# Performance work log

Hardware: AMD Instinct MI355X
Metric: run time of the kernel (lower is better)

Reference implementation:

```python
import jax, jax.numpy as jnp
import numpy as np

N = 200000   # num nodes
E = 2500000  # num edges
H = 32       # hidden_dim
EPS = 1e-5   # BatchNorm eps


def _gcn_conv(x, W, b, src, dst, norm):
    # GCNConv: D^{-1/2}(A+I)D^{-1/2} X W + b  (self-loops folded in via norm^2 term)
    h = x @ W                                   # [N, H_out]
    coef = norm[src] * norm[dst]                # [E]
    msg = h[src] * coef[:, None]                # [E, H_out] -- dominant HBM traffic
    agg = jax.ops.segment_sum(msg, dst, num_segments=N)
    agg = agg + h * (norm * norm)[:, None]      # self-loop contribution
    return agg + b


def _bn(x, gamma, beta):
    # BatchNorm1d in training mode: batch statistics over the node dimension
    m = jnp.mean(x, axis=0)
    v = jnp.var(x, axis=0)
    return gamma * (x - m) * jax.lax.rsqrt(v + EPS) + beta


def setup_inputs() -> dict:
    key = jax.random.key(0)
    ks = jax.random.split(key, 12)
    x = jax.random.uniform(ks[0], (N, 1), dtype=jnp.float32) * 50.0  # degree-like feature
    edge_index = jax.random.randint(ks[1], (2, E), 0, N, dtype=jnp.int64)
    edge_attr = jax.random.normal(ks[2], (E,), dtype=jnp.float32)
    s = 0.1
    return {
        'x': x, 'edge_index': edge_index, 'edge_attr': edge_attr,
        'W1': jax.random.normal(ks[3], (1, H), dtype=jnp.float32) * s,
        'b1': jnp.zeros((H,), jnp.float32),
        'g1': jnp.ones((H,), jnp.float32), 'be1': jnp.zeros((H,), jnp.float32),
        'W2': jax.random.normal(ks[4], (H, H), dtype=jnp.float32) * s,
        'b2': jnp.zeros((H,), jnp.float32),
        'g2': jnp.ones((H,), jnp.float32), 'be2': jnp.zeros((H,), jnp.float32),
        'W3': jax.random.normal(ks[5], (H, H), dtype=jnp.float32) * s,
        'b3': jnp.zeros((H,), jnp.float32),
        'g3': jnp.ones((H,), jnp.float32), 'be3': jnp.zeros((H,), jnp.float32),
        'fcW': jax.random.normal(ks[6], (H, 1), dtype=jnp.float32) * s,
        'fcb': jnp.zeros((1,), jnp.float32),
    }


def reference(x, edge_index, edge_attr, W1, b1, g1, be1, W2, b2, g2, be2,
              W3, b3, g3, be3, fcW, fcb):
    src, dst = edge_index[0], edge_index[1]
    # symmetric normalization from degrees of A + I
    deg = jax.ops.segment_sum(jnp.ones((E,), x.dtype), dst, num_segments=N) + 1.0
    norm = jax.lax.rsqrt(deg)                   # deg^{-1/2}, [N]

    h = jax.nn.relu(_bn(_gcn_conv(x, W1, b1, src, dst, norm), g1, be1))
    h = jax.nn.relu(_bn(_gcn_conv(h, W2, b2, src, dst, norm), g2, be2))
    h = jax.nn.relu(_bn(_gcn_conv(h, W3, b3, src, dst, norm), g3, be3))
    # dropout is identity in eval / deterministic reference
    return h @ fcW + fcb                        # [N, 1]
```

## Files before the change

kernel.cpp:

```cpp
#include <hip/hip_runtime.h>
#include <hip/hip_bf16.h>
#include <hip/hip_fp16.h>

#define N_NODES 200000
#define N_EDGES 2500000
#define HID 32
#define BN_EPS 1e-5f

#define BKT_SHIFT 10
#define B_BKT ((N_NODES + 1023) / 1024)
#define PAD 16
#define CAPB 14336
#define EDGES_PER_BLK 8192
#define NB_SCAT ((N_EDGES + EDGES_PER_BLK - 1) / EDGES_PER_BLK)

#define SBANK 4096
#define SSTR 16
#define S1SUM 0
#define S1SQ  16
#define L2SUM 32
#define L2SQ  544
#define L3SUM 1056
#define L3SQ  1568

#define NBN32 6250
#define NBL2  3125
#define ITL2  2
#define NBH   3125

typedef float nfloat4 __attribute__((ext_vector_type(4)));

__device__ __forceinline__ void atomAddF(float* p, float v) {
    unsafeAtomicAdd(p, v);
}

__device__ __forceinline__ void ntStore4(float* p, float a, float b, float c, float d) {
    nfloat4 v = {a, b, c, d};
    __builtin_nontemporal_store(v, (nfloat4*)p);
}

__global__ void k_init(int* __restrict__ bcur16, float* __restrict__ stats) {
    int i = blockIdx.x * blockDim.x + threadIdx.x;
    if (i < B_BKT * PAD) bcur16[i] = 0;
    if (i < 4 * SBANK) stats[i] = 0.0f;
}

__global__ void __launch_bounds__(1024)
k_scatter(const int* __restrict__ ei, int* __restrict__ bcur16,
          unsigned int* __restrict__ ebuf) {
    __shared__ int lh[B_BKT], lbase[B_BKT], lc[B_BKT];
    int t = threadIdx.x;
    if (t < B_BKT) { lh[t] = 0; lc[t] = 0; }
    __syncthreads();
    int base = blockIdx.x * EDGES_PER_BLK;
    int sv[8], dv[8];
#pragma unroll
    for (int k = 0; k < 8; k++) {
        int e = base + k * 1024 + t;
        if (e < N_EDGES) {
            sv[k] = ei[e];
            dv[k] = ei[N_EDGES + e];
            atomicAdd(&lh[dv[k] >> BKT_SHIFT], 1);
        } else dv[k] = -1;
    }
    __syncthreads();
    if (t < B_BKT) lbase[t] = lh[t] ? atomicAdd(&bcur16[t * PAD], lh[t]) : 0;
    __syncthreads();
#pragma unroll
    for (int k = 0; k < 8; k++) {
        if (dv[k] >= 0) {
            int b = dv[k] >> BKT_SHIFT;
            int loc = atomicAdd(&lc[b], 1);
            ebuf[(size_t)b * CAPB + lbase[b] + loc] =
                ((unsigned)(dv[k] & 1023) << 18) | (unsigned)sv[k];
        }
    }
}

__global__ void __launch_bounds__(1024)
k_bucket(const unsigned int* __restrict__ ebuf, const int* __restrict__ bcur16,
         const float* __restrict__ x, int* __restrict__ rowbeg,
         int* __restrict__ cntg, float* __restrict__ norm,
         float* __restrict__ xp, int* __restrict__ csrc) {
    __shared__ int hist[1024], rbase[1024];
    __shared__ int wsum[16];
    int b = blockIdx.x;
    int t = threadIdx.x;
    int lane = t & 63, wv = t >> 6;
    int count = bcur16[b * PAD];
    size_t ebase = (size_t)b * CAPB;
    int nbase = b << BKT_SHIFT;
    hist[t] = 0;
    __syncthreads();
    for (int i = t; i < count; i += 1024)
        atomicAdd(&hist[ebuf[ebase + i] >> 18], 1);
    __syncthreads();
    int v = hist[t];
    int val = v;
#pragma unroll
    for (int off = 1; off < 64; off <<= 1) {
        int nn = __shfl_up(val, off);
        if (lane >= off) val += nn;
    }
    if (lane == 63) wsum[wv] = val;
    __syncthreads();
    if (t < 16) {
        int wval = wsum[t];
        int wincl = wval;
#pragma unroll
        for (int off = 1; off < 16; off <<= 1) {
            int nn = __shfl_up(wincl, off, 16);
            if (t >= off) wincl += nn;
        }
        wsum[t] = wincl - wval;
    }
    __syncthreads();
    int excl = (val - v) + wsum[wv];
    int rb = b * CAPB + excl;
    rbase[t] = rb;
    int n = nbase + t;
    if (n < N_NODES) {
        rowbeg[n] = rb;
        cntg[n] = v;
        float nm = rsqrtf((float)v + 1.0f);
        norm[n] = nm;
        xp[n] = x[n] * nm;
    }
    __syncthreads();
    hist[t] = 0;
    __syncthreads();
    for (int i = t; i < count; i += 1024) {
        unsigned int w = ebuf[ebase + i];
        int ld = w >> 18;
        int loc = atomicAdd(&hist[ld], 1);
        csrc[rbase[ld] + loc] = (int)(w & 0x3FFFFu);
    }
}

__global__ void __launch_bounds__(256)
k_gather1(const int* __restrict__ rowbeg, const int* __restrict__ cntg,
          const int* __restrict__ csrc, const float* __restrict__ xp,
          const float* __restrict__ norm, float2* __restrict__ sn2,
          float* __restrict__ stats) {
    __shared__ float ls[256], lq[256];
    int tid = threadIdx.x;
    int nl = tid >> 3, q = tid & 7;
    int n = blockIdx.x * 32 + nl;
    int beg = rowbeg[n], dg = cntg[n];
    float A0 = 0.f, A1 = 0.f;
    int i = q;
    for (; i + 8 < dg; i += 16) {
        A0 += xp[__builtin_nontemporal_load(csrc + beg + i)];
        A1 += xp[__builtin_nontemporal_load(csrc + beg + i + 8)];
    }
    if (i < dg) A0 += xp[__builtin_nontemporal_load(csrc + beg + i)];
    float acc = A0 + A1;
    acc += __shfl_xor(acc, 1);
    acc += __shfl_xor(acc, 2);
    acc += __shfl_xor(acc, 4);
    float val = 0.f;
    if (q == 0) {
        acc += xp[n];
        float nm = norm[n];
        val = nm * acc;
        sn2[n] = make_float2(val, nm);
    }
    ls[tid] = val; lq[tid] = val * val;
    __syncthreads();
    for (int off = 128; off; off >>= 1) {
        if (tid < (unsigned)off) { ls[tid] += ls[tid + off]; lq[tid] += lq[tid + off]; }
        __syncthreads();
    }
    if (tid == 0) {
        int bo = (blockIdx.x & 3) * SBANK;
        atomAddF(&stats[bo + S1SUM], ls[0]);
        atomAddF(&stats[bo + S1SQ],  lq[0]);
    }
}

#define PHI(aa, bb, pp) ((pp).y * fmaxf(fmaf((aa), (pp).x, (bb)), 0.f))

__global__ void __launch_bounds__(256)
k_layer2(const int* __restrict__ rowbeg, const int* __restrict__ cntg,
         const int* __restrict__ csrc, const float2* __restrict__ sn2,
         const float* __restrict__ stats, const float* __restrict__ W1,
         const float* __restrict__ g1, const float* __restrict__ be1,
         const float* __restrict__ W2, float* __restrict__ B,
         float* __restrict__ sumO, float* __restrict__ sqO) {
    __shared__ float w2s[1024];
    __shared__ __align__(16) float ajs[32], bjs[32];
    __shared__ float yx[32][36];
    __shared__ float red[4][8][8];
    int tid = threadIdx.x;
    for (int i = tid; i < 1024; i += 256) w2s[i] = W2[i];
    if (tid < 32) {
        float sm = stats[S1SUM] + stats[SBANK + S1SUM] +
                   stats[2*SBANK + S1SUM] + stats[3*SBANK + S1SUM];
        float sq = stats[S1SQ] + stats[SBANK + S1SQ] +
                   stats[2*SBANK + S1SQ] + stats[3*SBANK + S1SQ];
        float m   = sm * (1.0f / N_NODES);
        float var = sq * (1.0f / N_NODES) - m * m;
        float w = W1[tid];
        float a = g1[tid] * w * rsqrtf(var * w * w + BN_EPS);
        ajs[tid] = a;
        bjs[tid] = be1[tid] - m * a;
    }
    __syncthreads();
    int nl = tid >> 3, cg = (tid & 7) * 4;
    float a0 = ajs[cg], a1 = ajs[cg+1], a2 = ajs[cg+2], a3 = ajs[cg+3];
    float b0 = bjs[cg], b1 = bjs[cg+1], b2 = bjs[cg+2], b3 = bjs[cg+3];
    float s0=0,s1=0,s2=0,s3=0,q0=0,q1=0,q2=0,q3=0;
#pragma unroll
    for (int it = 0; it < ITL2; it++) {
        int n = (it * NBL2 + blockIdx.x) * 32 + nl;
        int beg = rowbeg[n], dg = cntg[n];
        float2 self = sn2[n];
        float nm = self.y;
        float h0 = PHI(a0,b0,self), h1 = PHI(a1,b1,self),
              h2 = PHI(a2,b2,self), h3 = PHI(a3,b3,self);
        int i = 0;
        for (; i + 3 < dg; i += 4) {
            int e0 = __builtin_nontemporal_load(csrc + beg + i);
            int e1 = __builtin_nontemporal_load(csrc + beg + i + 1);
            int e2 = __builtin_nontemporal_load(csrc + beg + i + 2);
            int e3 = __builtin_nontemporal_load(csrc + beg + i + 3);
            float2 p0 = sn2[e0], p1 = sn2[e1], p2 = sn2[e2], p3 = sn2[e3];
            h0 += PHI(a0,b0,p0) + PHI(a0,b0,p1) + PHI(a0,b0,p2) + PHI(a0,b0,p3);
            h1 += PHI(a1,b1,p0) + PHI(a1,b1,p1) + PHI(a1,b1,p2) + PHI(a1,b1,p3);
            h2 += PHI(a2,b2,p0) + PHI(a2,b2,p1) + PHI(a2,b2,p2) + PHI(a2,b2,p3);
            h3 += PHI(a3,b3,p0) + PHI(a3,b3,p1) + PHI(a3,b3,p2) + PHI(a3,b3,p3);
        }
        for (; i < dg; i++) {
            float2 p = sn2[__builtin_nontemporal_load(csrc + beg + i)];
            h0 += PHI(a0,b0,p); h1 += PHI(a1,b1,p);
            h2 += PHI(a2,b2,p); h3 += PHI(a3,b3,p);
        }
        __syncthreads();
        *(float4*)&yx[nl][cg] = make_float4(h0,h1,h2,h3);
        __syncthreads();
        float o0=0,o1=0,o2=0,o3=0;
#pragma unroll
        for (int k = 0; k < 32; k += 4) {
            float4 hh  = *(const float4*)&yx[nl][k];
            float4 wr0 = *(const float4*)&w2s[(k+0)*32 + cg];
            float4 wr1 = *(const float4*)&w2s[(k+1)*32 + cg];
            float4 wr2 = *(const float4*)&w2s[(k+2)*32 + cg];
            float4 wr3 = *(const float4*)&w2s[(k+3)*32 + cg];
            o0 = fmaf(hh.x,wr0.x, fmaf(hh.y,wr1.x, fmaf(hh.z,wr2.x, fmaf(hh.w,wr3.x, o0))));
            o1 = fmaf(hh.x,wr0.y, fmaf(hh.y,wr1.y, fmaf(hh.z,wr2.y, fmaf(hh.w,wr3.y, o1))));
            o2 = fmaf(hh.x,wr0.z, fmaf(hh.y,wr1.z, fmaf(hh.z,wr2.z, fmaf(hh.w,wr3.z, o2))));
            o3 = fmaf(hh.x,wr0.w, fmaf(hh.y,wr1.w, fmaf(hh.z,wr2.w, fmaf(hh.w,wr3.w, o3))));
        }
        o0 *= nm; o1 *= nm; o2 *= nm; o3 *= nm;
        ntStore4(B + (size_t)n * 32 + cg, o0, o1, o2, o3);
        s0 += o0; s1 += o1; s2 += o2; s3 += o3;
        q0 += o0*o0; q1 += o1*o1; q2 += o2*o2; q3 += o3*o3;
    }
#pragma unroll
    for (int mask = 32; mask >= 8; mask >>= 1) {
        s0 += __shfl_xor(s0, mask); s1 += __shfl_xor(s1, mask);
        s2 += __shfl_xor(s2, mask); s3 += __shfl_xor(s3, mask);
        q0 += __shfl_xor(q0, mask); q1 += __shfl_xor(q1, mask);
        q2 += __shfl_xor(q2, mask); q3 += __shfl_xor(q3, mask);
    }
    int wv = tid >> 6, ln = tid & 63;
    if (ln < 8) {
        float* r = red[wv][ln];
        r[0]=s0; r[1]=s1; r[2]=s2; r[3]=s3;
        r[4]=q0; r[5]=q1; r[6]=q2; r[7]=q3;
    }
    __syncthreads();
    if (tid < 8) {
        float tacc[8] = {0,0,0,0,0,0,0,0};
#pragma unroll
        for (int w = 0; w < 4; w++)
#pragma unroll
            for (int k = 0; k < 8; k++) tacc[k] += red[w][tid][k];
        int cb = tid * 4;
        int bo = (blockIdx.x & 3) * SBANK;
#pragma unroll
        for (int k = 0; k < 4; k++) {
            atomAddF(&sumO[bo + (cb + k) * SSTR], tacc[k]);
            atomAddF(&sqO [bo + (cb + k) * SSTR], tacc[4 + k]);
        }
    }
}

__global__ void __launch_bounds__(256)
k_fusedB(const float* __restrict__ norm, const float* __restrict__ sum,
         const float* __restrict__ sumsq, const float* __restrict__ g,
         const float* __restrict__ be, const float* __restrict__ W,
         const float* __restrict__ aggIn, __half* __restrict__ hOut) {
    __shared__ float wl[1024];
    __shared__ float scs[32], shs[32];
    __shared__ float yx[32][36];
    int tid = threadIdx.x;
    for (int i = tid; i < 1024; i += 256) wl[i] = W[i];
    if (tid < 32) {
        int o = tid * SSTR;
        float sm = sum[o] + sum[o+SBANK] + sum[o+2*SBANK] + sum[o+3*SBANK];
        float sq = sumsq[o] + sumsq[o+SBANK] + sumsq[o+2*SBANK] + sumsq[o+3*SBANK];
        float m   = sm * (1.0f / N_NODES);
        float var = sq * (1.0f / N_NODES) - m * m;
        float scj = g[tid] * rsqrtf(var + BN_EPS);
        scs[tid] = scj;
        shs[tid] = be[tid] - m * scj;
    }
    __syncthreads();
    int nl = tid >> 3, cg = (tid & 7) * 4;
    int n = blockIdx.x * 32 + nl;
    float4 bi = *(const float4*)(aggIn + (size_t)n * 32 + cg);
    float y0 = fmaxf(scs[cg  ]*bi.x + shs[cg  ], 0.f);
    float y1 = fmaxf(scs[cg+1]*bi.y + shs[cg+1], 0.f);
    float y2 = fmaxf(scs[cg+2]*bi.z + shs[cg+2], 0.f);
    float y3 = fmaxf(scs[cg+3]*bi.w + shs[cg+3], 0.f);
    *(float4*)&yx[nl][cg] = make_float4(y0,y1,y2,y3);
    __syncthreads();
    float o0=0,o1=0,o2=0,o3=0;
#pragma unroll
    for (int k = 0; k < 32; k += 4) {
        float4 hh  = *(const float4*)&yx[nl][k];
        float4 wr0 = *(const float4*)&wl[(k+0)*32 + cg];
        float4 wr1 = *(const float4*)&wl[(k+1)*32 + cg];
        float4 wr2 = *(const float4*)&wl[(k+2)*32 + cg];
        float4 wr3 = *(const float4*)&wl[(k+3)*32 + cg];
        o0 = fmaf(hh.x,wr0.x, fmaf(hh.y,wr1.x, fmaf(hh.z,wr2.x, fmaf(hh.w,wr3.x, o0))));
        o1 = fmaf(hh.x,wr0.y, fmaf(hh.y,wr1.y, fmaf(hh.z,wr2.y, fmaf(hh.w,wr3.y, o1))));
        o2 = fmaf(hh.x,wr0.z, fmaf(hh.y,wr1.z, fmaf(hh.z,wr2.z, fmaf(hh.w,wr3.z, o2))));
        o3 = fmaf(hh.x,wr0.w, fmaf(hh.y,wr1.w, fmaf(hh.z,wr2.w, fmaf(hh.w,wr3.w, o3))));
    }
    float nm = norm[n];
    __half2 ha = __floats2half2_rn(o0 * nm, o1 * nm);
    __half2 hb = __floats2half2_rn(o2 * nm, o3 * nm);
    float2 pk;
    ((__half2*)&pk)[0] = ha;
    ((__half2*)&pk)[1] = hb;
    *(float2*)(hOut + (size_t)n * 32 + cg) = pk;
}

__device__ __forceinline__ void acc8(float* a, float4 raw) {
    const __half2* h = (const __half2*)&raw;
    float2 f0 = __half22float2(h[0]);
    float2 f1 = __half22float2(h[1]);
    float2 f2 = __half22float2(h[2]);
    float2 f3 = __half22float2(h[3]);
    a[0] += f0.x; a[1] += f0.y; a[2] += f1.x; a[3] += f1.y;
    a[4] += f2.x; a[5] += f2.y; a[6] += f3.x; a[7] += f3.y;
}

__device__ __forceinline__ void acc8m(float* a, float4 raw, float m) {
    const __half2* h = (const __half2*)&raw;
    float2 f0 = __half22float2(h[0]);
    float2 f1 = __half22float2(h[1]);
    float2 f2 = __half22float2(h[2]);
    float2 f3 = __half22float2(h[3]);
    a[0] = fmaf(m, f0.x, a[0]); a[1] = fmaf(m, f0.y, a[1]);
    a[2] = fmaf(m, f1.x, a[2]); a[3] = fmaf(m, f1.y, a[3]);
    a[4] = fmaf(m, f2.x, a[4]); a[5] = fmaf(m, f2.y, a[5]);
    a[6] = fmaf(m, f3.x, a[6]); a[7] = fmaf(m, f3.y, a[7]);
}

__global__ void __launch_bounds__(256)
k_gatherH(const int* __restrict__ rowbeg, const int* __restrict__ cntg,
          const int* __restrict__ csrc, const __half* __restrict__ A,
          const float* __restrict__ norm, float* __restrict__ B,
          float* __restrict__ sum, float* __restrict__ sumsq) {
    int tid = threadIdx.x;
    int nl = tid >> 2;
    int c8 = (tid & 3) * 8;
    int n = blockIdx.x * 64 + nl;
    int beg = rowbeg[n], dg = cntg[n];
    const __half* Ac = A + c8;
    float acc[8] = {0,0,0,0,0,0,0,0};
    acc8(acc, *(const float4*)(Ac + (size_t)n * 32));
    int iters = (dg + 7) >> 3;
    for (int t = 0; t < iters; t++) {
        int i0 = t * 8;
        int e[8]; float m[8];
#pragma unroll
        for (int j = 0; j < 8; j++) {
            int idx = i0 + j;
            bool ok = idx < dg;
            int ic = ok ? idx : dg - 1;
            e[j] = __builtin_nontemporal_load(csrc + beg + ic);
            m[j] = ok ? 1.f : 0.f;
        }
        float4 r0 = *(const float4*)(Ac + (size_t)e[0] * 32);
        float4 r1 = *(const float4*)(Ac + (size_t)e[1] * 32);
        float4 r2 = *(const float4*)(Ac + (size_t)e[2] * 32);
        float4 r3 = *(const float4*)(Ac + (size_t)e[3] * 32);
        float4 r4 = *(const float4*)(Ac + (size_t)e[4] * 32);
        float4 r5 = *(const float4*)(Ac + (size_t)e[5] * 32);
        float4 r6 = *(const float4*)(Ac + (size_t)e[6] * 32);
        float4 r7 = *(const float4*)(Ac + (size_t)e[7] * 32);
        acc8m(acc, r0, m[0]); acc8m(acc, r1, m[1]);
        acc8m(acc, r2, m[2]); acc8m(acc, r3, m[3]);
        acc8m(acc, r4, m[4]); acc8m(acc, r5, m[5]);
        acc8m(acc, r6, m[6]); acc8m(acc, r7, m[7]);
    }
    float nm = norm[n];
    float o[8];
#pragma unroll
    for (int k = 0; k < 8; k++) o[k] = acc[k] * nm;
    ntStore4(B + (size_t)n * 32 + c8,     o[0], o[1], o[2], o[3]);
    ntStore4(B + (size_t)n * 32 + c8 + 4, o[4], o[5], o[6], o[7]);
    float st[16];
#pragma unroll
    for (int k = 0; k < 8; k++) { st[k] = o[k]; st[8 + k] = o[k] * o[k]; }
#pragma unroll
    for (int mask = 32; mask >= 4; mask >>= 1)
#pragma unroll
        for (int k = 0; k < 16; k++) st[k] += __shfl_xor(st[k], mask);
    __shared__ float red[4][4][16];
    int wv = tid >> 6, ln = tid & 63;
    if (ln < 4) {
#pragma unroll
        for (int k = 0; k < 16; k++) red[wv][ln][k] = st[k];
    }
    __syncthreads();
    if (tid < 4) {
        float tacc[16];
#pragma unroll
        for (int k = 0; k < 16; k++) tacc[k] = 0.f;
#pragma unroll
        for (int w = 0; w < 4; w++)
#pragma unroll
            for (int k = 0; k < 16; k++) tacc[k] += red[w][tid][k];
        int cb = tid * 8;
        int bo = (blockIdx.x & 3) * SBANK;
#pragma unroll
        for (int k = 0; k < 8; k++) {
            atomAddF(&sum[bo + (cb + k) * SSTR], tacc[k]);
            atomAddF(&sumsq[bo + (cb + k) * SSTR], tacc[8 + k]);
        }
    }
}

__global__ void __launch_bounds__(256)
k_final(const float* __restrict__ aggIn, const float* __restrict__ sum,
        const float* __restrict__ sumsq, const float* __restrict__ g,
        const float* __restrict__ be, const float* __restrict__ fcW,
        const float* __restrict__ fcb, float* __restrict__ out) {
    __shared__ float scs[32], shs[32], fws[32];
    int tid = threadIdx.x;
    if (tid < 32) {
        int o = tid * SSTR;
        float sm = sum[o] + sum[o+SBANK] + sum[o+2*SBANK] + sum[o+3*SBANK];
        float sq = sumsq[o] + sumsq[o+SBANK] + sumsq[o+2*SBANK] + sumsq[o+3*SBANK];
        float m   = sm * (1.0f / N_NODES);
        float var = sq * (1.0f / N_NODES) - m * m;
        float scj = g[tid] * rsqrtf(var + BN_EPS);
        scs[tid] = scj;
        shs[tid] = be[tid] - m * scj;
        fws[tid] = fcW[tid];
    }
    __syncthreads();
    int nl = tid >> 3, cg = (tid & 7) * 4;
    int n = blockIdx.x * 32 + nl;
    float4 bi = *(const float4*)(aggIn + (size_t)n * 32 + cg);
    float v = fmaxf(scs[cg  ]*bi.x + shs[cg  ], 0.f) * fws[cg  ]
            + fmaxf(scs[cg+1]*bi.y + shs[cg+1], 0.f) * fws[cg+1]
            + fmaxf(scs[cg+2]*bi.z + shs[cg+2], 0.f) * fws[cg+2]
            + fmaxf(scs[cg+3]*bi.w + shs[cg+3], 0.f) * fws[cg+3];
    v += __shfl_xor(v, 1);
    v += __shfl_xor(v, 2);
    v += __shfl_xor(v, 4);
    if ((tid & 7) == 0) out[n] = v + fcb[0];
}

extern "C" void kernel_launch(void* const* d_in, const int* in_sizes, int n_in,
                              void* d_out, int out_size, void* d_ws, size_t ws_size,
                              hipStream_t stream) {
    const float* x   = (const float*)d_in[0];
    const int*   ei  = (const int*)d_in[1];
    const float* W1  = (const float*)d_in[3];
    const float* g1  = (const float*)d_in[5];
    const float* be1 = (const float*)d_in[6];
    const float* W2  = (const float*)d_in[7];
    const float* g2  = (const float*)d_in[9];
    const float* be2 = (const float*)d_in[10];
    const float* W3  = (const float*)d_in[11];
    const float* g3  = (const float*)d_in[13];
    const float* be3 = (const float*)d_in[14];
    const float* fcW = (const float*)d_in[15];
    const float* fcb = (const float*)d_in[16];
    float* out = (float*)d_out;

    char* base = (char*)d_ws;
    __half*       A16  = (__half*)base;
    unsigned int* ebuf = (unsigned int*)base;
    float*  B      = (float*)(base + (size_t)N_NODES * 32 * 4);
    int*    csrc   = (int*)(base + (size_t)N_NODES * 32 * 8);
    int*    rowbeg = csrc + (size_t)B_BKT * CAPB;
    int*    cntg   = rowbeg + N_NODES;
    float*  norm   = (float*)(cntg + N_NODES);
    float*  xp     = norm + N_NODES;
    float2* sn2    = (float2*)(xp + N_NODES);
    float*  stats  = (float*)(sn2 + N_NODES);
    int*    bcur16 = (int*)(stats + 4 * SBANK);

    k_init   <<<64, 256, 0, stream>>>(bcur16, stats);
    k_scatter<<<NB_SCAT, 1024, 0, stream>>>(ei, bcur16, ebuf);
    k_bucket <<<B_BKT, 1024, 0, stream>>>(ebuf, bcur16, x, rowbeg, cntg, norm, xp, csrc);
    k_gather1<<<NBN32, 256, 0, stream>>>(rowbeg, cntg, csrc, xp, norm, sn2, stats);
    k_layer2 <<<NBL2, 256, 0, stream>>>(rowbeg, cntg, csrc, sn2, stats,
                                        W1, g1, be1, W2, B,
                                        stats + L2SUM, stats + L2SQ);
    k_fusedB <<<NBN32, 256, 0, stream>>>(norm, stats + L2SUM, stats + L2SQ,
                                         g2, be2, W3, B, A16);
    k_gatherH<<<NBH, 256, 0, stream>>>(rowbeg, cntg, csrc, A16, norm, B,
                                       stats + L3SUM, stats + L3SQ);
    k_final  <<<NBN32, 256, 0, stream>>>(B, stats + L3SUM, stats + L3SQ,
                                         g3, be3, fcW, fcb, out);
}
```

Measured before the change: 314.6 us.

## Halve bucket size, cache edges in registers, split layer2 neighbor loop across two threads

The CSR build now uses 512-node buckets with 512-thread blocks. Each thread keeps its up to 15 bucket edges in registers, so the packed edge buffer is read once instead of twice. In layer 2, each node gets 16 threads instead of 8: the two halves take alternating groups of 4 neighbors and split the 32x32 matmul, then combine results with cross-lane shuffles. This adds parallelism for the gather-bound aggregation and shortens per-thread dependency chains, at the cost of extra shuffles, more blocks and more buckets.

```diff
diff --git a/kernel.cpp b/kernel.cpp
--- a/kernel.cpp
+++ b/kernel.cpp
@@ -7,10 +7,11 @@
 #define HID 32
 #define BN_EPS 1e-5f
 
-#define BKT_SHIFT 10
-#define B_BKT ((N_NODES + 1023) / 1024)
+#define BKT_SHIFT 9
+#define B_BKT ((N_NODES + 511) / 512)
 #define PAD 16
-#define CAPB 14336
+#define CAPB 7680
+#define EPT 15
 #define EDGES_PER_BLK 8192
 #define NB_SCAT ((N_EDGES + EDGES_PER_BLK - 1) / EDGES_PER_BLK)
 
@@ -24,7 +25,7 @@
 #define L3SQ  1568
 
 #define NBN32 6250
-#define NBL2  3125
+#define NBL2  6250
 #define ITL2  2
 #define NBH   3125
 
@@ -72,18 +73,18 @@
             int b = dv[k] >> BKT_SHIFT;
             int loc = atomicAdd(&lc[b], 1);
             ebuf[(size_t)b * CAPB + lbase[b] + loc] =
-                ((unsigned)(dv[k] & 1023) << 18) | (unsigned)sv[k];
-        }
-    }
-}
-
-__global__ void __launch_bounds__(1024)
+                ((unsigned)(dv[k] & 511) << 18) | (unsigned)sv[k];
+        }
+    }
+}
+
+__global__ void __launch_bounds__(512)
 k_bucket(const unsigned int* __restrict__ ebuf, const int* __restrict__ bcur16,
          const float* __restrict__ x, int* __restrict__ rowbeg,
          int* __restrict__ cntg, float* __restrict__ norm,
          float* __restrict__ xp, int* __restrict__ csrc) {
-    __shared__ int hist[1024], rbase[1024];
-    __shared__ int wsum[16];
+    __shared__ int hist[512], rbase[512];
+    __shared__ int wsum[8];
     int b = blockIdx.x;
     int t = threadIdx.x;
     int lane = t & 63, wv = t >> 6;
@@ -92,8 +93,15 @@
     int nbase = b << BKT_SHIFT;
     hist[t] = 0;
     __syncthreads();
-    for (int i = t; i < count; i += 1024)
-        atomicAdd(&hist[ebuf[ebase + i] >> 18], 1);
+    unsigned int ev[EPT];
+#pragma unroll
+    for (int k = 0; k < EPT; k++) {
+        int i = t + k * 512;
+        ev[k] = (i < count) ? ebuf[ebase + i] : 0u;
+    }
+#pragma unroll
+    for (int k = 0; k < EPT; k++)
+        if (t + k * 512 < count) atomicAdd(&hist[ev[k] >> 18], 1);
     __syncthreads();
     int v = hist[t];
     int val = v;
@@ -104,12 +112,12 @@
     }
     if (lane == 63) wsum[wv] = val;
     __syncthreads();
-    if (t < 16) {
+    if (t < 8) {
         int wval = wsum[t];
         int wincl = wval;
 #pragma unroll
-        for (int off = 1; off < 16; off <<= 1) {
-            int nn = __shfl_up(wincl, off, 16);
+        for (int off = 1; off < 8; off <<= 1) {
+            int nn = __shfl_up(wincl, off, 8);
             if (t >= off) wincl += nn;
         }
         wsum[t] = wincl - wval;
@@ -129,11 +137,13 @@
     __syncthreads();
     hist[t] = 0;
     __syncthreads();
-    for (int i = t; i < count; i += 1024) {
-        unsigned int w = ebuf[ebase + i];
-        int ld = w >> 18;
-        int loc = atomicAdd(&hist[ld], 1);
-        csrc[rbase[ld] + loc] = (int)(w & 0x3FFFFu);
+#pragma unroll
+    for (int k = 0; k < EPT; k++) {
+        if (t + k * 512 < count) {
+            int ld = ev[k] >> 18;
+            int loc = atomicAdd(&hist[ld], 1);
+            csrc[rbase[ld] + loc] = (int)(ev[k] & 0x3FFFFu);
+        }
     }
 }
 
@@ -189,7 +199,7 @@
          float* __restrict__ sumO, float* __restrict__ sqO) {
     __shared__ float w2s[1024];
     __shared__ __align__(16) float ajs[32], bjs[32];
-    __shared__ float yx[32][36];
+    __shared__ float yx[16][36];
     __shared__ float red[4][8][8];
     int tid = threadIdx.x;
     for (int i = tid; i < 1024; i += 256) w2s[i] = W2[i];
@@ -206,41 +216,54 @@
         bjs[tid] = be1[tid] - m * a;
     }
     __syncthreads();
-    int nl = tid >> 3, cg = (tid & 7) * 4;
+    int nl = tid >> 4;
+    int t16 = tid & 15;
+    int cg = (t16 & 7) * 4;
+    int half = t16 >> 3;
     float a0 = ajs[cg], a1 = ajs[cg+1], a2 = ajs[cg+2], a3 = ajs[cg+3];
     float b0 = bjs[cg], b1 = bjs[cg+1], b2 = bjs[cg+2], b3 = bjs[cg+3];
     float s0=0,s1=0,s2=0,s3=0,q0=0,q1=0,q2=0,q3=0;
 #pragma unroll
     for (int it = 0; it < ITL2; it++) {
-        int n = (it * NBL2 + blockIdx.x) * 32 + nl;
+        int n = (it * NBL2 + blockIdx.x) * 16 + nl;
         int beg = rowbeg[n], dg = cntg[n];
         float2 self = sn2[n];
         float nm = self.y;
-        float h0 = PHI(a0,b0,self), h1 = PHI(a1,b1,self),
-              h2 = PHI(a2,b2,self), h3 = PHI(a3,b3,self);
-        int i = 0;
-        for (; i + 3 < dg; i += 4) {
-            int e0 = __builtin_nontemporal_load(csrc + beg + i);
-            int e1 = __builtin_nontemporal_load(csrc + beg + i + 1);
-            int e2 = __builtin_nontemporal_load(csrc + beg + i + 2);
-            int e3 = __builtin_nontemporal_load(csrc + beg + i + 3);
+        float h0, h1, h2, h3;
+        if (half == 0) {
+            h0 = PHI(a0,b0,self); h1 = PHI(a1,b1,self);
+            h2 = PHI(a2,b2,self); h3 = PHI(a3,b3,self);
+        } else { h0 = h1 = h2 = h3 = 0.f; }
+        int Q = dg >> 2;
+        for (int q = half; q < Q; q += 2) {
+            int i = beg + q * 4;
+            int e0 = __builtin_nontemporal_load(csrc + i);
+            int e1 = __builtin_nontemporal_load(csrc + i + 1);
+            int e2 = __builtin_nontemporal_load(csrc + i + 2);
+            int e3 = __builtin_nontemporal_load(csrc + i + 3);
             float2 p0 = sn2[e0], p1 = sn2[e1], p2 = sn2[e2], p3 = sn2[e3];
             h0 += PHI(a0,b0,p0) + PHI(a0,b0,p1) + PHI(a0,b0,p2) + PHI(a0,b0,p3);
             h1 += PHI(a1,b1,p0) + PHI(a1,b1,p1) + PHI(a1,b1,p2) + PHI(a1,b1,p3);
             h2 += PHI(a2,b2,p0) + PHI(a2,b2,p1) + PHI(a2,b2,p2) + PHI(a2,b2,p3);
             h3 += PHI(a3,b3,p0) + PHI(a3,b3,p1) + PHI(a3,b3,p2) + PHI(a3,b3,p3);
         }
-        for (; i < dg; i++) {
-            float2 p = sn2[__builtin_nontemporal_load(csrc + beg + i)];
-            h0 += PHI(a0,b0,p); h1 += PHI(a1,b1,p);
-            h2 += PHI(a2,b2,p); h3 += PHI(a3,b3,p);
-        }
+        if ((Q & 1) == half) {
+            for (int i = beg + Q * 4; i < beg + dg; i++) {
+                float2 p = sn2[__builtin_nontemporal_load(csrc + i)];
+                h0 += PHI(a0,b0,p); h1 += PHI(a1,b1,p);
+                h2 += PHI(a2,b2,p); h3 += PHI(a3,b3,p);
+            }
+        }
+        h0 += __shfl_xor(h0, 8); h1 += __shfl_xor(h1, 8);
+        h2 += __shfl_xor(h2, 8); h3 += __shfl_xor(h3, 8);
         __syncthreads();
-        *(float4*)&yx[nl][cg] = make_float4(h0,h1,h2,h3);
+        if (half == 0) *(float4*)&yx[nl][cg] = make_float4(h0,h1,h2,h3);
         __syncthreads();
         float o0=0,o1=0,o2=0,o3=0;
-#pragma unroll
-        for (int k = 0; k < 32; k += 4) {
+        int k0 = half * 16;
+#pragma unroll
+        for (int kk = 0; kk < 16; kk += 4) {
+            int k = k0 + kk;
             float4 hh  = *(const float4*)&yx[nl][k];
             float4 wr0 = *(const float4*)&w2s[(k+0)*32 + cg];
             float4 wr1 = *(const float4*)&w2s[(k+1)*32 + cg];
@@ -251,10 +274,14 @@
             o2 = fmaf(hh.x,wr0.z, fmaf(hh.y,wr1.z, fmaf(hh.z,wr2.z, fmaf(hh.w,wr3.z, o2))));
             o3 = fmaf(hh.x,wr0.w, fmaf(hh.y,wr1.w, fmaf(hh.z,wr2.w, fmaf(hh.w,wr3.w, o3))));
         }
-        o0 *= nm; o1 *= nm; o2 *= nm; o3 *= nm;
-        ntStore4(B + (size_t)n * 32 + cg, o0, o1, o2, o3);
-        s0 += o0; s1 += o1; s2 += o2; s3 += o3;
-        q0 += o0*o0; q1 += o1*o1; q2 += o2*o2; q3 += o3*o3;
+        o0 += __shfl_xor(o0, 8); o1 += __shfl_xor(o1, 8);
+        o2 += __shfl_xor(o2, 8); o3 += __shfl_xor(o3, 8);
+        if (half == 0) {
+            o0 *= nm; o1 *= nm; o2 *= nm; o3 *= nm;
+            ntStore4(B + (size_t)n * 32 + cg, o0, o1, o2, o3);
+            s0 += o0; s1 += o1; s2 += o2; s3 += o3;
+            q0 += o0*o0; q1 += o1*o1; q2 += o2*o2; q3 += o3*o3;
+        }
     }
 #pragma unroll
     for (int mask = 32; mask >= 8; mask >>= 1) {
@@ -501,7 +528,7 @@
 
     k_init   <<<64, 256, 0, stream>>>(bcur16, stats);
     k_scatter<<<NB_SCAT, 1024, 0, stream>>>(ei, bcur16, ebuf);
-    k_bucket <<<B_BKT, 1024, 0, stream>>>(ebuf, bcur16, x, rowbeg, cntg, norm, xp, csrc);
+    k_bucket <<<B_BKT, 512, 0, stream>>>(ebuf, bcur16, x, rowbeg, cntg, norm, xp, csrc);
     k_gather1<<<NBN32, 256, 0, stream>>>(rowbeg, cntg, csrc, xp, norm, sn2, stats);
     k_layer2 <<<NBL2, 256, 0, stream>>>(rowbeg, cntg, csrc, sn2, stats,
                                         W1, g1, be1, W2, B,
```

Measured after the change: 360.2 us. 1.15x slower.
